# Performance work log

Hardware: AMD Instinct MI355X
Metric: run time of the kernel (lower is better)

The kernel has to match this reference:

```python
import jax, jax.numpy as jnp
import numpy as np

B, S, SE, D, H, F1, I, E, ND = 8, 512, 512, 1024, 16, 4096, 1024, 8, 4

def _ln(x, g, b, eps=1e-5):
    mu = x.mean(-1, keepdims=True)
    var = ((x - mu) ** 2).mean(-1, keepdims=True)
    return (x - mu) * jax.lax.rsqrt(var + eps) * g + b

def _mha(q_in, kv_in, qw, qb, kw, kb, vw, vb, ow, ob):
    b, sq, d = q_in.shape
    sk = kv_in.shape[1]
    dh = d // H
    scale = dh ** -0.5
    q = ((q_in @ qw.T + qb) * scale).reshape(b, sq, H, dh)
    k = (kv_in @ kw.T + kb).reshape(b, sk, H, dh)
    v = (kv_in @ vw.T + vb).reshape(b, sk, H, dh)
    attn = jax.nn.softmax(jnp.einsum('bqhd,bkhd->bhqk', q, k), axis=-1)
    o = jnp.einsum('bhqk,bkhd->bqhd', attn, v).reshape(b, sq, d)
    return o @ ow.T + ob

def setup_inputs():
    key = jax.random.key(0)
    ks = jax.random.split(key, 40)
    p = lambda i, sh: jax.random.normal(ks[i], sh, jnp.float32) * 0.02
    return {
        'hidden_states': jax.random.normal(ks[0], (B, S, D), jnp.float32),
        'encoder_hidden_states': jax.random.normal(ks[1], (B, SE, D), jnp.float32),
        'idxes': jax.random.randint(ks[2], (B,), 0, ND),
        'sa_qw': p(3, (D, D)), 'sa_qb': p(4, (D,)), 'sa_kw': p(5, (D, D)), 'sa_kb': p(6, (D,)),
        'sa_vw': p(7, (D, D)), 'sa_vb': p(8, (D,)), 'sa_ow': p(9, (D, D)), 'sa_ob': p(10, (D,)),
        'ca_qw': p(11, (D, D)), 'ca_qb': p(12, (D,)), 'ca_kw': p(13, (D, D)), 'ca_kb': p(14, (D,)),
        'ca_vw': p(15, (D, D)), 'ca_vb': p(16, (D,)), 'ca_ow': p(17, (D, D)), 'ca_ob': p(18, (D,)),
        'sa_ln_g': jnp.ones((D,), jnp.float32), 'sa_ln_b': jnp.zeros((D,), jnp.float32),
        'ca_ln_g': jnp.ones((D,), jnp.float32), 'ca_ln_b': jnp.zeros((D,), jnp.float32),
        'fin_ln_g': jnp.ones((D,), jnp.float32), 'fin_ln_b': jnp.zeros((D,), jnp.float32),
        'fc1_w': p(19, (F1, D)), 'fc1_b': p(20, (F1,)),
        'fc2_w': p(21, (D, F1)), 'fc2_b': p(22, (D,)),
        'exp1_w': p(23, (E, I, D)), 'exp1_b': p(24, (E, I)),
        'exp2_w': p(25, (E, D, I)),
        'gate_w': p(26, (ND, E, D)), 'gate_b': p(27, (ND, E)),
    }

def reference(hidden_states, encoder_hidden_states, idxes, sa_qw, sa_qb, sa_kw, sa_kb, sa_vw, sa_vb, sa_ow, sa_ob, ca_qw, ca_qb, ca_kw, ca_kb, ca_vw, ca_vb, ca_ow, ca_ob, sa_ln_g, sa_ln_b, ca_ln_g, ca_ln_b, fin_ln_g, fin_ln_b, fc1_w, fc1_b, fc2_w, fc2_b, exp1_w, exp1_b, exp2_w, gate_w, gate_b):
    # self-attention block
    res = hidden_states
    h = _mha(hidden_states, hidden_states, sa_qw, sa_qb, sa_kw, sa_kb, sa_vw, sa_vb, sa_ow, sa_ob)
    h = _ln(res + h, sa_ln_g, sa_ln_b)
    # cross-attention block
    res = h
    h = _mha(h, encoder_hidden_states, ca_qw, ca_qb, ca_kw, ca_kb, ca_vw, ca_vb, ca_ow, ca_ob)
    h = _ln(res + h, ca_ln_g, ca_ln_b)
    # dataset-gated MoE FFN (dropout=0 eval, margin_loss=False, keep_resident=True)
    bsz, seq, d = h.shape
    x = h.reshape(-1, d)                              # [T, D]
    tok_ds = jnp.repeat(idxes, seq)                   # [T] dataset id per token
    logits = jnp.einsum('ted,td->te', gate_w[tok_ds], x) + gate_b[tok_ds]
    probs = jax.nn.softmax(logits, axis=-1)
    gate = jnp.argmax(probs, axis=-1)                 # top-1 expert per token
    gate_value = jnp.max(probs, axis=-1)
    oh = jax.nn.one_hot(gate, E, dtype=x.dtype)       # [T, E] dispatch mask
    # effective expert fc1 = concat(fc1, expert_fc1): shared half + per-token expert half
    h1 = jax.nn.gelu(x @ fc1_w.T + fc1_b, approximate=False)                                  # [T, F1]
    h2 = jax.nn.gelu(jnp.einsum('td,te,eid->ti', x, oh, exp1_w) + exp1_b[gate], approximate=False)  # [T, I]
    # effective expert fc2 = concat(fc2, expert_fc2, dim=1), shared fc2 bias
    out = h1 @ fc2_w.T + jnp.einsum('ti,te,edi->td', h2, oh, exp2_w) + fc2_b                  # [T, D]
    out = out * gate_value[:, None]                   # keep_resident: scale before residual
    out = _ln(x + out, fin_ln_g, fin_ln_b)
    return out.reshape(bsz, seq, d)
```

## Files before the change

kernel.cpp:

```cpp
#include <hip/hip_runtime.h>
#include <math.h>

constexpr int cS = 512, cD = 1024, cH = 16, cDH = 64;
constexpr int cF1 = 4096, cI = 1024, cE = 8;
constexpr int cT = 4096;
constexpr long long TD = (long long)cT * cD;
constexpr long long WW = 1048576;

typedef __attribute__((ext_vector_type(8))) short bfrag;
typedef _Float16 f16x8 __attribute__((ext_vector_type(8)));
typedef __attribute__((ext_vector_type(4))) float f32x4;

__device__ __forceinline__ float gelu_exact(float x) {
  return 0.5f * x * (1.0f + erff(x * 0.70710678118654752440f));
}
__device__ __forceinline__ unsigned short f2b_rne(float x) {
  union { float f; unsigned u; } v; v.f = x;
  unsigned r = v.u + 0x7fffu + ((v.u >> 16) & 1u);
  return (unsigned short)(r >> 16);
}
__device__ __forceinline__ void split2(float v, unsigned short& h, unsigned short& m) {
  _Float16 hh = (_Float16)v;
  float r = v - (float)hh;
  _Float16 mm = (_Float16)r;
  union { _Float16 f; unsigned short u; } a, b;
  a.f = hh; b.f = mm;
  h = a.u; m = b.u;
}
__device__ __forceinline__ void async16(const void* g, void* l) {
  __builtin_amdgcn_global_load_lds(
      (const __attribute__((address_space(1))) unsigned int*)g,
      (__attribute__((address_space(3))) unsigned int*)l, 16, 0, 0);
}
__device__ __forceinline__ float wsum(float v) {
#pragma unroll
  for (int off = 32; off; off >>= 1) v += __shfl_xor(v, off, 64);
  return v;
}
__device__ __forceinline__ float wmax(float v) {
#pragma unroll
  for (int off = 32; off; off >>= 1) v = fmaxf(v, __shfl_xor(v, off, 64));
  return v;
}

template<int BM, int BN, int OUT_MODE>
__global__ __launch_bounds__(256) void mgemm2(
    const unsigned short* __restrict__ Ap, long long aPS, long long sA, int lda,
    const unsigned short* __restrict__ Bp, long long bPS, long long sB, int ldb,
    const float* __restrict__ bias,
    void* __restrict__ Cp, long long sC, int ldc,
    int K, float alpha, int zbase)
{
  constexpr int WM = BM / 2, WN = BN / 2, AI = WM / 16, BJ = WN / 16;
  constexpr int CA = 2 * (BM / 16);
  constexpr int CB = 2 * (BN / 16);
  constexpr int CTOT = CA + CB;
  static_assert(CTOT % 4 == 0, "chunk count");
  constexpr int NCH = CTOT / 4;
  constexpr int LT = (BM + BN) * 64;

  __shared__ unsigned short lds[2][LT];

  const int tid = threadIdx.x;
  const int w = tid >> 6, lane = tid & 63;
  const int z = blockIdx.z;
  const int m0 = blockIdx.x * BM, n0 = blockIdx.y * BN;
  const int wm = (w >> 1) * WM, wn = (w & 1) * WN;
  const int lr = lane >> 2, lc8 = (lane & 3) * 8;

  const unsigned short* gsrc[NCH];
  int loff[NCH];
#pragma unroll
  for (int ci = 0; ci < NCH; ++ci) {
    const int c = w + ci * 4;
    if (c < CA) {
      const int p = c / (BM / 16), cc = c % (BM / 16);
      const int row = cc * 16 + lr;
      gsrc[ci] = Ap + p * aPS + (long long)z * sA + (long long)(m0 + row) * lda + lc8;
      loff[ci] = p * (BM * 32) + cc * (16 * 32);
    } else {
      const int cb = c - CA;
      const int p = cb / (BN / 16), cc = cb % (BN / 16);
      const int row = cc * 16 + lr;
      gsrc[ci] = Bp + p * bPS + (long long)z * sB + (long long)(n0 + row) * ldb + lc8;
      loff[ci] = 2 * (BM * 32) + p * (BN * 32) + cc * (16 * 32);
    }
  }

  f32x4 acc[AI][BJ];
#pragma unroll
  for (int i = 0; i < AI; ++i)
#pragma unroll
    for (int j = 0; j < BJ; ++j) acc[i][j] = (f32x4){0.f, 0.f, 0.f, 0.f};

#pragma unroll
  for (int ci = 0; ci < NCH; ++ci) async16(gsrc[ci], &lds[0][loff[ci]]);
  __syncthreads();

  int cur = 0;
  for (int k0 = 32; k0 <= K; k0 += 32) {
    if (k0 < K) {
#pragma unroll
      for (int ci = 0; ci < NCH; ++ci) async16(gsrc[ci] + k0, &lds[cur ^ 1][loff[ci]]);
    }
    const unsigned short* LA0 = &lds[cur][0];
    const unsigned short* LA1 = &lds[cur][BM * 32];
    const unsigned short* LB0 = &lds[cur][2 * (BM * 32)];
    const unsigned short* LB1 = &lds[cur][2 * (BM * 32) + BN * 32];

    f16x8 bf0[BJ], bf1[BJ], af[AI];
#pragma unroll
    for (int j = 0; j < BJ; ++j) {
      bf0[j] = *(const f16x8*)&LB0[(wn + j * 16 + (lane & 15)) * 32 + (lane >> 4) * 8];
      bf1[j] = *(const f16x8*)&LB1[(wn + j * 16 + (lane & 15)) * 32 + (lane >> 4) * 8];
    }
#pragma unroll
    for (int i = 0; i < AI; ++i)
      af[i] = *(const f16x8*)&LA0[(wm + i * 16 + (lane & 15)) * 32 + (lane >> 4) * 8];
#pragma unroll
    for (int i = 0; i < AI; ++i)
#pragma unroll
      for (int j = 0; j < BJ; ++j)
        acc[i][j] = __builtin_amdgcn_mfma_f32_16x16x32_f16(af[i], bf0[j], acc[i][j], 0, 0, 0);
#pragma unroll
    for (int i = 0; i < AI; ++i)
#pragma unroll
      for (int j = 0; j < BJ; ++j)
        acc[i][j] = __builtin_amdgcn_mfma_f32_16x16x32_f16(af[i], bf1[j], acc[i][j], 0, 0, 0);
#pragma unroll
    for (int i = 0; i < AI; ++i)
      af[i] = *(const f16x8*)&LA1[(wm + i * 16 + (lane & 15)) * 32 + (lane >> 4) * 8];
#pragma unroll
    for (int i = 0; i < AI; ++i)
#pragma unroll
      for (int j = 0; j < BJ; ++j)
        acc[i][j] = __builtin_amdgcn_mfma_f32_16x16x32_f16(af[i], bf0[j], acc[i][j], 0, 0, 0);
    __syncthreads();
    cur ^= 1;
  }

  const int zz = zbase + z;
#pragma unroll
  for (int i = 0; i < AI; ++i) {
#pragma unroll
    for (int r = 0; r < 4; ++r) {
      const int gm = m0 + wm + i * 16 + (lane >> 4) * 4 + r;
#pragma unroll
      for (int j = 0; j < BJ; ++j) {
        const int gn = n0 + wn + j * 16 + (lane & 15);
        float v = acc[i][j][r];
        if constexpr (OUT_MODE == 4) {
          v += bias[zz * cD + gn];
          unsigned short* C = (unsigned short*)Cp + (long long)zz * 2 * TD;
          const int b = gm >> 9, s = gm & 511, h = gn >> 6, dd = gn & 63;
          const long long idx = (((long long)(b * cH + h) * cS + s) << 6) + dd;
          unsigned short h_, m_;
          split2(v, h_, m_);
          C[idx] = h_; C[TD + idx] = m_;
        } else if constexpr (OUT_MODE == 5) {
          const int b = zz >> 4, h = zz & 15;
          const long long idx = ((long long)(b * cS + gm) << 10) + h * 64 + gn;
          unsigned short h_, m_;
          split2(v, h_, m_);
          ((unsigned short*)Cp)[idx] = h_;
          ((unsigned short*)Cp)[sC + idx] = m_;
        } else {
          if (bias) v += bias[gn];
          v *= alpha;
          const long long idx = (long long)z * sC + (long long)gm * ldc + gn;
          ((float*)Cp)[idx] = v;
        }
      }
    }
  }
}

__global__ __launch_bounds__(256) void transposeV(
    const unsigned short* __restrict__ src, unsigned short* __restrict__ dst)
{
  __shared__ unsigned short t[128 * 64];
  const int st = blockIdx.x;
  const int bh = blockIdx.y;
  const long long pl = (long long)blockIdx.z * TD;
  const unsigned short* Sp = src + pl + ((long long)bh * cS + st * 128) * cDH;
  const int tid = threadIdx.x;
  const int r0 = tid >> 3, c0 = (tid & 7) * 8;
#pragma unroll
  for (int i = 0; i < 4; ++i) {
    const int r = r0 + i * 32;
    uint4 v = *(const uint4*)(Sp + (long long)r * cDH + c0);
    *(uint4*)&t[r * 64 + (c0 ^ ((r & 7) << 3))] = v;
  }
  __syncthreads();
  const int dd = tid >> 2;
  unsigned short* Dp = dst + pl + (long long)(bh * cDH + dd) * cS + st * 128;
#pragma unroll
  for (int i = 0; i < 4; ++i) {
    const int s0 = ((tid & 3) + i * 4) * 8;
    alignas(16) unsigned short v[8];
#pragma unroll
    for (int j = 0; j < 8; ++j)
      v[j] = t[(s0 + j) * 64 + (dd ^ (j << 3))];
    *(uint4*)(Dp + s0) = *(const uint4*)v;
  }
}

template<int GATHER>
__global__ __launch_bounds__(256) void mgemm1(
    const unsigned short* __restrict__ A, int lda,
    const unsigned short* __restrict__ Bw, long long sB, int ldb,
    const float* __restrict__ bias, int sBias,
    void* __restrict__ Cp, int ldc,
    int K, int act, int obf, int accum,
    const int* __restrict__ token_list, const int* __restrict__ offsets)
{
  int m0, n0, beg = 0, cnt = 0x7fffffff;
  long long boff = 0;
  if constexpr (GATHER) {
    const int e = blockIdx.y;
    beg = offsets[e]; cnt = offsets[e + 1] - beg;
    m0 = blockIdx.z * 128;
    if (m0 >= cnt) return;
    n0 = blockIdx.x * 128;
    boff = (long long)e * sB;
    if (bias) bias += (long long)e * sBias;
  } else {
    m0 = blockIdx.x * 128; n0 = blockIdx.y * 128;
  }
  __shared__ unsigned short lds[2][256 * 32];
  const int tid = threadIdx.x, w = tid >> 6, lane = tid & 63;
  const int wm = (w >> 1) * 64, wn = (w & 1) * 64;
  const int lr = lane >> 2, lc8 = (lane & 3) * 8;

  const unsigned short* gsrc[4];
  int loff[4];
#pragma unroll
  for (int ci = 0; ci < 4; ++ci) {
    const int c = w + ci * 4;
    if (c < 8) {
      const int row = c * 16 + lr;
      long long grow;
      if constexpr (GATHER) {
        int mr = m0 + row; if (mr >= cnt) mr = cnt - 1;
        grow = token_list[beg + mr];
      } else grow = m0 + row;
      gsrc[ci] = A + grow * (long long)lda + lc8;
      loff[ci] = c * (16 * 32);
    } else {
      const int cc = c - 8;
      const int row = cc * 16 + lr;
      gsrc[ci] = Bw + boff + (long long)(n0 + row) * ldb + lc8;
      loff[ci] = 128 * 32 + cc * (16 * 32);
    }
  }
  f32x4 acc[4][4];
#pragma unroll
  for (int i = 0; i < 4; ++i)
#pragma unroll
    for (int j = 0; j < 4; ++j) acc[i][j] = (f32x4){0.f, 0.f, 0.f, 0.f};

#pragma unroll
  for (int ci = 0; ci < 4; ++ci) async16(gsrc[ci], &lds[0][loff[ci]]);
  __syncthreads();

  int cur = 0;
  for (int k0 = 32; k0 <= K; k0 += 32) {
    if (k0 < K) {
#pragma unroll
      for (int ci = 0; ci < 4; ++ci) async16(gsrc[ci] + k0, &lds[cur ^ 1][loff[ci]]);
    }
    const unsigned short* lA = &lds[cur][0];
    const unsigned short* lB = &lds[cur][128 * 32];
    bfrag af[4], bf[4];
#pragma unroll
    for (int i = 0; i < 4; ++i)
      af[i] = *(const bfrag*)&lA[(wm + i * 16 + (lane & 15)) * 32 + (lane >> 4) * 8];
#pragma unroll
    for (int j = 0; j < 4; ++j)
      bf[j] = *(const bfrag*)&lB[(wn + j * 16 + (lane & 15)) * 32 + (lane >> 4) * 8];
#pragma unroll
    for (int i = 0; i < 4; ++i)
#pragma unroll
      for (int j = 0; j < 4; ++j)
        acc[i][j] = __builtin_amdgcn_mfma_f32_16x16x32_bf16(af[i], bf[j], acc[i][j], 0, 0, 0);
    __syncthreads();
    cur ^= 1;
  }

#pragma unroll
  for (int i = 0; i < 4; ++i) {
#pragma unroll
    for (int r = 0; r < 4; ++r) {
      const int ml = wm + i * 16 + (lane >> 4) * 4 + r;
      long long orow = 0; bool ok = true;
      if constexpr (GATHER) {
        if (m0 + ml < cnt) orow = token_list[beg + m0 + ml]; else ok = false;
      } else orow = m0 + ml;
      if (ok) {
#pragma unroll
        for (int j = 0; j < 4; ++j) {
          const int gn = n0 + wn + j * 16 + (lane & 15);
          float v = acc[i][j][r];
          if (bias) v += bias[gn];
          if (act) v = gelu_exact(v);
          const long long idx = orow * (long long)ldc + gn;
          if (obf) ((unsigned short*)Cp)[idx] = f2b_rne(v);
          else if (accum) ((float*)Cp)[idx] += v;
          else ((float*)Cp)[idx] = v;
        }
      }
    }
  }
}

__global__ __launch_bounds__(256) void softmax2(
    const float* __restrict__ Sc, unsigned short* __restrict__ P, long long pPS)
{
  const int w = threadIdx.x >> 6, lane = threadIdx.x & 63;
  const long long row = (long long)blockIdx.x * 4 + w;
  const float* pr = Sc + row * cS + lane * 8;
  float4 a = *(const float4*)pr;
  float4 b = *(const float4*)(pr + 4);
  float e[8] = {a.x, a.y, a.z, a.w, b.x, b.y, b.z, b.w};
  float m = e[0];
#pragma unroll
  for (int q = 1; q < 8; ++q) m = fmaxf(m, e[q]);
  m = wmax(m);
  float s = 0.f;
#pragma unroll
  for (int q = 0; q < 8; ++q) { e[q] = expf(e[q] - m); s += e[q]; }
  s = wsum(s);
  const float inv = 1.0f / s;
  unsigned h[4], mm[4];
#pragma unroll
  for (int q = 0; q < 4; ++q) {
    unsigned short h0, m0s, h1, m1s;
    split2(e[2 * q] * inv, h0, m0s);
    split2(e[2 * q + 1] * inv, h1, m1s);
    h[q] = (unsigned)h0 | ((unsigned)h1 << 16);
    mm[q] = (unsigned)m0s | ((unsigned)m1s << 16);
  }
  const long long o = row * cS + lane * 8;
  *(uint4*)&P[o] = *(const uint4*)h;
  *(uint4*)&P[pPS + o] = *(const uint4*)mm;
}

__global__ __launch_bounds__(256) void addln_kernel(
    const float* __restrict__ ra, const float* __restrict__ rb,
    const float* __restrict__ rowscale,
    const float* __restrict__ g, const float* __restrict__ be,
    float* __restrict__ out, unsigned short* __restrict__ out16,
    unsigned short* __restrict__ out2p,
    int gate_on, const int* __restrict__ idxes,
    const float* __restrict__ gw, const float* __restrict__ gb,
    int* __restrict__ gate_idx, float* __restrict__ gate_val, int* __restrict__ counts)
{
  const int w = threadIdx.x >> 6, lane = threadIdx.x & 63;
  const int row = blockIdx.x * 4 + w;
  const long long base = (long long)row * cD + lane * 16;
  const float sc = rowscale ? rowscale[row] : 1.0f;
  float v[16];
#pragma unroll
  for (int q = 0; q < 4; ++q) {
    float4 a = *(const float4*)(ra + base + q * 4);
    float4 b = *(const float4*)(rb + base + q * 4);
    v[q * 4 + 0] = a.x + b.x * sc; v[q * 4 + 1] = a.y + b.y * sc;
    v[q * 4 + 2] = a.z + b.z * sc; v[q * 4 + 3] = a.w + b.w * sc;
  }
  float s = 0.f;
#pragma unroll
  for (int q = 0; q < 16; ++q) s += v[q];
  const float mu = wsum(s) * (1.0f / cD);
  float vp = 0.f;
#pragma unroll
  for (int q = 0; q < 16; ++q) { float c = v[q] - mu; vp += c * c; }
  const float rstd = 1.0f / sqrtf(wsum(vp) * (1.0f / cD) + 1e-5f);
  float x[16];
#pragma unroll
  for (int q = 0; q < 4; ++q) {
    float4 gv = *(const float4*)(g + lane * 16 + q * 4);
    float4 bv = *(const float4*)(be + lane * 16 + q * 4);
    x[q * 4 + 0] = (v[q * 4 + 0] - mu) * rstd * gv.x + bv.x;
    x[q * 4 + 1] = (v[q * 4 + 1] - mu) * rstd * gv.y + bv.y;
    x[q * 4 + 2] = (v[q * 4 + 2] - mu) * rstd * gv.z + bv.z;
    x[q * 4 + 3] = (v[q * 4 + 3] - mu) * rstd * gv.w + bv.w;
  }
  if (out) {
#pragma unroll
    for (int q = 0; q < 4; ++q) {
      float4 o; o.x = x[q * 4]; o.y = x[q * 4 + 1]; o.z = x[q * 4 + 2]; o.w = x[q * 4 + 3];
      *(float4*)(out + base + q * 4) = o;
    }
  }
  if (out16) {
    unsigned u[8];
#pragma unroll
    for (int q = 0; q < 8; ++q)
      u[q] = (unsigned)f2b_rne(x[2 * q]) | ((unsigned)f2b_rne(x[2 * q + 1]) << 16);
    *(uint4*)&out16[base] = *(const uint4*)&u[0];
    *(uint4*)&out16[base + 8] = *(const uint4*)&u[4];
  }
  if (out2p) {
    unsigned uh[8], um[8];
#pragma unroll
    for (int q = 0; q < 8; ++q) {
      unsigned short h0, m0s, h1, m1s;
      split2(x[2 * q], h0, m0s);
      split2(x[2 * q + 1], h1, m1s);
      uh[q] = (unsigned)h0 | ((unsigned)h1 << 16);
      um[q] = (unsigned)m0s | ((unsigned)m1s << 16);
    }
    *(uint4*)&out2p[base] = *(const uint4*)&uh[0];
    *(uint4*)&out2p[base + 8] = *(const uint4*)&uh[4];
    *(uint4*)&out2p[TD + base] = *(const uint4*)&um[0];
    *(uint4*)&out2p[TD + base + 8] = *(const uint4*)&um[4];
  }
  if (gate_on) {
    const int ds = idxes[row >> 9];
    const float* gwr = gw + (long long)ds * (cE * cD) + lane * 16;
    float glog[8];
#pragma unroll
    for (int e = 0; e < 8; ++e) {
      float pe = 0.f;
#pragma unroll
      for (int q = 0; q < 4; ++q) {
        float4 wv = *(const float4*)(gwr + e * cD + q * 4);
        pe += x[q * 4] * wv.x + x[q * 4 + 1] * wv.y + x[q * 4 + 2] * wv.z + x[q * 4 + 3] * wv.w;
      }
      glog[e] = wsum(pe);
    }
    if (lane == 0) {
      float m = glog[0] + gb[ds * cE];
      int arg = 0;
      float gl[8];
      gl[0] = m;
#pragma unroll
      for (int e = 1; e < 8; ++e) {
        gl[e] = glog[e] + gb[ds * cE + e];
        if (gl[e] > m) { m = gl[e]; arg = e; }
      }
      float ssum = 0.f;
#pragma unroll
      for (int e = 0; e < 8; ++e) ssum += expf(gl[e] - m);
      gate_idx[row] = arg;
      gate_val[row] = 1.0f / ssum;
      atomicAdd(&counts[arg], 1);
    }
  }
}

__global__ __launch_bounds__(256) void conv2x4(
    const float* s0, const float* s1, const float* s2, const float* s3,
    unsigned short* dst, int n, float sc0)
{
  const int wsel = blockIdx.y;
  const float* s = (wsel == 0) ? s0 : (wsel == 1) ? s1 : (wsel == 2) ? s2 : s3;
  const float sc = (wsel == 0) ? sc0 : 1.0f;
  unsigned short* d = dst + (long long)wsel * 2 * n;
  const long long i = ((long long)blockIdx.x * 256 + threadIdx.x) * 4;
  if (i >= n) return;
  float4 v = *(const float4*)(s + i);
  float vv[4] = {v.x * sc, v.y * sc, v.z * sc, v.w * sc};
  unsigned short h[4], m[4];
#pragma unroll
  for (int q = 0; q < 4; ++q) split2(vv[q], h[q], m[q]);
  uint2 u;
  u.x = (unsigned)h[0] | ((unsigned)h[1] << 16); u.y = (unsigned)h[2] | ((unsigned)h[3] << 16);
  *(uint2*)&d[i] = u;
  u.x = (unsigned)m[0] | ((unsigned)m[1] << 16); u.y = (unsigned)m[2] | ((unsigned)m[3] << 16);
  *(uint2*)&d[n + i] = u;
}

__global__ __launch_bounds__(256) void conv2p(const float* __restrict__ s,
                                              unsigned short* __restrict__ d, long long n)
{
  const long long i = ((long long)blockIdx.x * 256 + threadIdx.x) * 4;
  if (i >= n) return;
  float4 v = *(const float4*)(s + i);
  unsigned short h[4], m[4];
  split2(v.x, h[0], m[0]); split2(v.y, h[1], m[1]);
  split2(v.z, h[2], m[2]); split2(v.w, h[3], m[3]);
  uint2 u;
  u.x = (unsigned)h[0] | ((unsigned)h[1] << 16); u.y = (unsigned)h[2] | ((unsigned)h[3] << 16);
  *(uint2*)&d[i] = u;
  u.x = (unsigned)m[0] | ((unsigned)m[1] << 16); u.y = (unsigned)m[2] | ((unsigned)m[3] << 16);
  *(uint2*)&d[n + i] = u;
}

__global__ __launch_bounds__(256) void conv1(const float* __restrict__ s,
                                             unsigned short* __restrict__ d, long long n)
{
  const long long i = ((long long)blockIdx.x * 256 + threadIdx.x) * 4;
  if (i >= n) return;
  float4 v = *(const float4*)(s + i);
  uint2 u;
  u.x = (unsigned)f2b_rne(v.x) | ((unsigned)f2b_rne(v.y) << 16);
  u.y = (unsigned)f2b_rne(v.z) | ((unsigned)f2b_rne(v.w) << 16);
  *(uint2*)&d[i] = u;
}

__global__ void prep_bias(const float* a0, const float* a1, const float* a2,
                          const float* b0, const float* b1, const float* b2,
                          float* dst)
{
  const int i = blockIdx.x * 256 + threadIdx.x;
  const int seg = i >> 10, off = i & 1023;
  const float* srcs[6] = {a0, a1, a2, b0, b1, b2};
  const float sc = (seg == 0 || seg == 3) ? 0.125f : 1.0f;
  dst[i] = srcs[seg][off] * sc;
}

__global__ void scan_kernel(const int* __restrict__ counts, int* __restrict__ offsets,
                            int* __restrict__ cursor)
{
  if (threadIdx.x == 0 && blockIdx.x == 0) {
    int a = 0;
    for (int e = 0; e < cE; ++e) { offsets[e] = a; cursor[e] = a; a += counts[e]; }
    offsets[cE] = a;
  }
}

__global__ __launch_bounds__(256) void scatter_kernel(
    const int* __restrict__ gate_idx, int* __restrict__ cursor, int* __restrict__ token_list)
{
  int t = blockIdx.x * 256 + threadIdx.x;
  if (t < cT) {
    int e = gate_idx[t];
    int slot = atomicAdd(&cursor[e], 1);
    token_list[slot] = t;
  }
}

extern "C" void kernel_launch(void* const* d_in, const int* in_sizes, int n_in,
                              void* d_out, int out_size, void* d_ws, size_t ws_size,
                              hipStream_t stream)
{
  (void)in_sizes; (void)n_in; (void)out_size;
  const float* hidden  = (const float*)d_in[0];
  const float* encoder = (const float*)d_in[1];
  const int*   idxes   = (const int*)d_in[2];
  const float* sa_qw = (const float*)d_in[3];
  const float* sa_qb = (const float*)d_in[4];
  const float* sa_kw = (const float*)d_in[5];
  const float* sa_kb = (const float*)d_in[6];
  const float* sa_vw = (const float*)d_in[7];
  const float* sa_vb = (const float*)d_in[8];
  const float* sa_ow = (const float*)d_in[9];
  const float* sa_ob = (const float*)d_in[10];
  const float* ca_qw = (const float*)d_in[11];
  const float* ca_qb = (const float*)d_in[12];
  const float* ca_kw = (const float*)d_in[13];
  const float* ca_kb = (const float*)d_in[14];
  const float* ca_vw = (const float*)d_in[15];
  const float* ca_vb = (const float*)d_in[16];
  const float* ca_ow = (const float*)d_in[17];
  const float* ca_ob = (const float*)d_in[18];
  const float* sa_ln_g = (const float*)d_in[19];
  const float* sa_ln_b = (const float*)d_in[20];
  const float* ca_ln_g = (const float*)d_in[21];
  const float* ca_ln_b = (const float*)d_in[22];
  const float* fin_ln_g = (const float*)d_in[23];
  const float* fin_ln_b = (const float*)d_in[24];
  const float* fc1_w = (const float*)d_in[25];
  const float* fc1_b = (const float*)d_in[26];
  const float* fc2_w = (const float*)d_in[27];
  const float* fc2_b = (const float*)d_in[28];
  const float* exp1_w = (const float*)d_in[29];
  const float* exp1_b = (const float*)d_in[30];
  const float* exp2_w = (const float*)d_in[31];
  const float* gate_w = (const float*)d_in[32];
  const float* gate_b = (const float*)d_in[33];
  float* out = (float*)d_out;

  size_t off = 0;
  auto alloc = [&](size_t bytes) {
    void* p = (char*)d_ws + off;
    off += (bytes + 255) & ~(size_t)255;
    return p;
  };
  unsigned short* wbuf = (unsigned short*)alloc(4ll * 2 * WW * 2);
  unsigned short* QKVs = (unsigned short*)alloc(4ll * 2 * TD * 2);
  unsigned short* attnO16 = (unsigned short*)alloc(2ll * TD * 2);
  float* hsa   = (float*)alloc(TD * 4);
  float* biasb = (float*)alloc(6 * cD * 4);
  float* gate_val = (float*)alloc(cT * 4);
  int* gate_idx   = (int*)alloc(cT * 4);
  int* token_list = (int*)alloc(cT * 4);
  int* ctl        = (int*)alloc(64 * 4);
  int* counts  = ctl;
  int* offsets = ctl + 16;
  int* cursor  = ctl + 32;
  const size_t off_x = off;
  float* xbuf = (float*)alloc(TD * 4);
  unsigned short* x16 = (unsigned short*)alloc(TD * 2);

  long long region_bytes = (long long)ws_size - (long long)off_x;
  long long perz = (long long)cS * cS * 8;
  int ZB = (int)(region_bytes / perz);
  if (ZB < 1) ZB = 1;
  if (ZB > 128) ZB = 128;
  float* scoresF = (float*)((char*)d_ws + off_x);
  unsigned short* Pp = (unsigned short*)((char*)d_ws + off_x + (long long)ZB * cS * cS * 4);
  const long long pPS = (long long)ZB * cS * cS;

  unsigned short* A16 = QKVs + 6 * TD;
  unsigned short* hsa16 = attnO16;
  float* OdeltaF = (float*)QKVs;
  unsigned short* h1 = attnO16;
  unsigned short* h2 = QKVs;
  float* moeF = (float*)(QKVs + 2 * WW * 4);

  dim3 blk(256);
  hipMemsetAsync(counts, 0, cE * sizeof(int), stream);
  prep_bias<<<dim3(24), blk, 0, stream>>>(sa_qb, sa_kb, sa_vb, ca_qb, ca_kb, ca_vb, biasb);

  auto attention = [&]() {
    for (int zb = 0; zb < 128; zb += ZB) {
      int zc = 128 - zb; if (zc > ZB) zc = ZB;
      mgemm2<128, 64, 0><<<dim3(4, 8, zc), blk, 0, stream>>>(
          QKVs + (long long)zb * (cS * cDH), TD, (long long)cS * cDH, cDH,
          QKVs + 2 * TD + (long long)zb * (cS * cDH), TD, (long long)cS * cDH, cDH,
          nullptr, scoresF, (long long)cS * cS, cS, cDH, 1.0f, 0);
      softmax2<<<dim3(zc * cS / 4), blk, 0, stream>>>(scoresF, Pp, pPS);
      mgemm2<128, 64, 5><<<dim3(4, 1, zc), blk, 0, stream>>>(
          Pp, pPS, (long long)cS * cS, cS,
          QKVs + 6 * TD + (long long)zb * (cDH * cS), TD, (long long)cDH * cS, cS,
          nullptr, attnO16, TD, 0, cS, 1.0f, zb);
    }
  };

  conv2x4<<<dim3(1024, 4), blk, 0, stream>>>(sa_qw, sa_kw, sa_vw, sa_ow, wbuf, (int)WW, 0.125f);
  conv2p<<<dim3(4096), blk, 0, stream>>>(hidden, A16, TD);
  mgemm2<64, 128, 4><<<dim3(64, 8, 3), blk, 0, stream>>>(
      A16, TD, 0, cD, wbuf, WW, 2 * WW, cD,
      biasb, QKVs, 0, 0, cD, 1.0f, 0);
  transposeV<<<dim3(4, 128, 2), blk, 0, stream>>>(QKVs + 4 * TD, QKVs + 6 * TD);
  attention();
  mgemm2<64, 128, 0><<<dim3(64, 8, 1), blk, 0, stream>>>(
      attnO16, TD, 0, cD, wbuf + 6ll * WW, WW, 0, cD,
      sa_ob, OdeltaF, 0, cD, cD, 1.0f, 0);
  addln_kernel<<<dim3(cT / 4), blk, 0, stream>>>(
      hidden, OdeltaF, nullptr, sa_ln_g, sa_ln_b, hsa, nullptr, hsa16,
      0, nullptr, nullptr, nullptr, nullptr, nullptr, nullptr);

  conv2x4<<<dim3(1024, 4), blk, 0, stream>>>(ca_qw, ca_kw, ca_vw, ca_ow, wbuf, (int)WW, 0.125f);
  mgemm2<64, 128, 4><<<dim3(64, 8, 1), blk, 0, stream>>>(
      hsa16, TD, 0, cD, wbuf, WW, 2 * WW, cD,
      biasb + 3 * cD, QKVs, 0, 0, cD, 1.0f, 0);
  conv2p<<<dim3(4096), blk, 0, stream>>>(encoder, A16, TD);
  mgemm2<64, 128, 4><<<dim3(64, 8, 2), blk, 0, stream>>>(
      A16, TD, 0, cD, wbuf + 2ll * WW, WW, 2 * WW, cD,
      biasb + 3 * cD, QKVs, 0, 0, cD, 1.0f, 1);
  transposeV<<<dim3(4, 128, 2), blk, 0, stream>>>(QKVs + 4 * TD, QKVs + 6 * TD);
  attention();
  mgemm2<64, 128, 0><<<dim3(64, 8, 1), blk, 0, stream>>>(
      attnO16, TD, 0, cD, wbuf + 6ll * WW, WW, 0, cD,
      ca_ob, OdeltaF, 0, cD, cD, 1.0f, 0);
  addln_kernel<<<dim3(cT / 4), blk, 0, stream>>>(
      hsa, OdeltaF, nullptr, ca_ln_g, ca_ln_b, xbuf, x16, nullptr,
      1, idxes, gate_w, gate_b, gate_idx, gate_val, counts);

  scan_kernel<<<dim3(1), dim3(64), 0, stream>>>(counts, offsets, cursor);
  scatter_kernel<<<dim3(16), blk, 0, stream>>>(gate_idx, cursor, token_list);

  unsigned short* wfc1 = wbuf;
  unsigned short* wfc2 = wbuf + 4194304;
  conv1<<<dim3(4096), blk, 0, stream>>>(fc1_w, wfc1, 4194304);
  conv1<<<dim3(4096), blk, 0, stream>>>(fc2_w, wfc2, 4194304);
  for (int tc = 0; tc < cT; tc += 2048) {
    mgemm1<0><<<dim3(16, 32), blk, 0, stream>>>(
        x16 + (long long)tc * cD, cD, wfc1, 0, cD, fc1_b, 0,
        h1, cF1, cD, 1, 1, 0, nullptr, nullptr);
    mgemm1<0><<<dim3(16, 8), blk, 0, stream>>>(
        h1, cF1, wfc2, 0, cF1, fc2_b, 0,
        moeF + (long long)tc * cD, cD, cF1, 0, 0, 0, nullptr, nullptr);
  }
  conv1<<<dim3(8192), blk, 0, stream>>>(exp1_w, wbuf, 8388608);
  mgemm1<1><<<dim3(8, 8, 32), blk, 0, stream>>>(
      x16, cD, wbuf, (long long)cI * cD, cD, exp1_b, cI,
      h2, cI, cD, 1, 1, 0, token_list, offsets);
  conv1<<<dim3(8192), blk, 0, stream>>>(exp2_w, wbuf, 8388608);
  mgemm1<1><<<dim3(8, 8, 32), blk, 0, stream>>>(
      h2, cI, wbuf, (long long)cD * cI, cI, nullptr, 0,
      moeF, cD, cI, 0, 0, 1, token_list, offsets);

  addln_kernel<<<dim3(cT / 4), blk, 0, stream>>>(
      xbuf, moeF, gate_val, fin_ln_g, fin_ln_b, out, nullptr, nullptr,
      0, nullptr, nullptr, nullptr, nullptr, nullptr, nullptr);
}
```

Measured before the change: 1.207 ms.

## Generalize GEMM warp layout, enlarge tiles, and run FFN in one pass

Adds template parameters for warp count and warp-row arrangement to the split-precision GEMM kernel. Projection GEMMs switch to larger tiles, including 128x256 tiles with 512-thread blocks, and the QK^T scores GEMM uses 64x256 tiles. The point is to raise data reuse per block and cut the number of launched blocks. The shared FFN is no longer chunked in two 2048-token passes; it runs as a single pass with h1 moved to a larger buffer region, which adds memory-footprint risk if that region overlaps other live data.

```diff
diff --git a/kernel.cpp b/kernel.cpp
--- a/kernel.cpp
+++ b/kernel.cpp
@@ -43,20 +43,21 @@
   return v;
 }
 
-template<int BM, int BN, int OUT_MODE>
-__global__ __launch_bounds__(256) void mgemm2(
+template<int BM, int BN, int NW, int WR, int OUT_MODE>
+__global__ __launch_bounds__(NW * 64) void mgemm2(
     const unsigned short* __restrict__ Ap, long long aPS, long long sA, int lda,
     const unsigned short* __restrict__ Bp, long long bPS, long long sB, int ldb,
     const float* __restrict__ bias,
     void* __restrict__ Cp, long long sC, int ldc,
     int K, float alpha, int zbase)
 {
-  constexpr int WM = BM / 2, WN = BN / 2, AI = WM / 16, BJ = WN / 16;
+  constexpr int WC = NW / WR;
+  constexpr int WM = BM / WR, WN = BN / WC, AI = WM / 16, BJ = WN / 16;
   constexpr int CA = 2 * (BM / 16);
   constexpr int CB = 2 * (BN / 16);
   constexpr int CTOT = CA + CB;
-  static_assert(CTOT % 4 == 0, "chunk count");
-  constexpr int NCH = CTOT / 4;
+  static_assert(CTOT % NW == 0, "chunk count");
+  constexpr int NCH = CTOT / NW;
   constexpr int LT = (BM + BN) * 64;
 
   __shared__ unsigned short lds[2][LT];
@@ -65,14 +66,14 @@
   const int w = tid >> 6, lane = tid & 63;
   const int z = blockIdx.z;
   const int m0 = blockIdx.x * BM, n0 = blockIdx.y * BN;
-  const int wm = (w >> 1) * WM, wn = (w & 1) * WN;
+  const int wm = (w / WC) * WM, wn = (w % WC) * WN;
   const int lr = lane >> 2, lc8 = (lane & 3) * 8;
 
   const unsigned short* gsrc[NCH];
   int loff[NCH];
 #pragma unroll
   for (int ci = 0; ci < NCH; ++ci) {
-    const int c = w + ci * 4;
+    const int c = w + ci * NW;
     if (c < CA) {
       const int p = c / (BM / 16), cc = c % (BM / 16);
       const int row = cc * 16 + lr;
@@ -606,23 +607,23 @@
   unsigned short* A16 = QKVs + 6 * TD;
   unsigned short* hsa16 = attnO16;
   float* OdeltaF = (float*)QKVs;
-  unsigned short* h1 = attnO16;
   unsigned short* h2 = QKVs;
   float* moeF = (float*)(QKVs + 2 * WW * 4);
-
-  dim3 blk(256);
+  unsigned short* h1 = QKVs + 16ll * WW;
+
+  dim3 blk(256), blk512(512);
   hipMemsetAsync(counts, 0, cE * sizeof(int), stream);
   prep_bias<<<dim3(24), blk, 0, stream>>>(sa_qb, sa_kb, sa_vb, ca_qb, ca_kb, ca_vb, biasb);
 
   auto attention = [&]() {
     for (int zb = 0; zb < 128; zb += ZB) {
       int zc = 128 - zb; if (zc > ZB) zc = ZB;
-      mgemm2<128, 64, 0><<<dim3(4, 8, zc), blk, 0, stream>>>(
+      mgemm2<64, 256, 4, 1, 0><<<dim3(8, 2, zc), blk, 0, stream>>>(
           QKVs + (long long)zb * (cS * cDH), TD, (long long)cS * cDH, cDH,
           QKVs + 2 * TD + (long long)zb * (cS * cDH), TD, (long long)cS * cDH, cDH,
           nullptr, scoresF, (long long)cS * cS, cS, cDH, 1.0f, 0);
       softmax2<<<dim3(zc * cS / 4), blk, 0, stream>>>(scoresF, Pp, pPS);
-      mgemm2<128, 64, 5><<<dim3(4, 1, zc), blk, 0, stream>>>(
+      mgemm2<128, 64, 4, 2, 5><<<dim3(4, 1, zc), blk, 0, stream>>>(
           Pp, pPS, (long long)cS * cS, cS,
           QKVs + 6 * TD + (long long)zb * (cDH * cS), TD, (long long)cDH * cS, cS,
           nullptr, attnO16, TD, 0, cS, 1.0f, zb);
@@ -631,12 +632,12 @@
 
   conv2x4<<<dim3(1024, 4), blk, 0, stream>>>(sa_qw, sa_kw, sa_vw, sa_ow, wbuf, (int)WW, 0.125f);
   conv2p<<<dim3(4096), blk, 0, stream>>>(hidden, A16, TD);
-  mgemm2<64, 128, 4><<<dim3(64, 8, 3), blk, 0, stream>>>(
+  mgemm2<128, 256, 8, 2, 4><<<dim3(32, 4, 3), blk512, 0, stream>>>(
       A16, TD, 0, cD, wbuf, WW, 2 * WW, cD,
       biasb, QKVs, 0, 0, cD, 1.0f, 0);
   transposeV<<<dim3(4, 128, 2), blk, 0, stream>>>(QKVs + 4 * TD, QKVs + 6 * TD);
   attention();
-  mgemm2<64, 128, 0><<<dim3(64, 8, 1), blk, 0, stream>>>(
+  mgemm2<64, 256, 4, 1, 0><<<dim3(64, 4, 1), blk, 0, stream>>>(
       attnO16, TD, 0, cD, wbuf + 6ll * WW, WW, 0, cD,
       sa_ob, OdeltaF, 0, cD, cD, 1.0f, 0);
   addln_kernel<<<dim3(cT / 4), blk, 0, stream>>>(
@@ -644,16 +645,16 @@
       0, nullptr, nullptr, nullptr, nullptr, nullptr, nullptr);
 
   conv2x4<<<dim3(1024, 4), blk, 0, stream>>>(ca_qw, ca_kw, ca_vw, ca_ow, wbuf, (int)WW, 0.125f);
-  mgemm2<64, 128, 4><<<dim3(64, 8, 1), blk, 0, stream>>>(
+  mgemm2<64, 256, 4, 1, 4><<<dim3(64, 4, 1), blk, 0, stream>>>(
       hsa16, TD, 0, cD, wbuf, WW, 2 * WW, cD,
       biasb + 3 * cD, QKVs, 0, 0, cD, 1.0f, 0);
   conv2p<<<dim3(4096), blk, 0, stream>>>(encoder, A16, TD);
-  mgemm2<64, 128, 4><<<dim3(64, 8, 2), blk, 0, stream>>>(
+  mgemm2<128, 256, 8, 2, 4><<<dim3(32, 4, 2), blk512, 0, stream>>>(
       A16, TD, 0, cD, wbuf + 2ll * WW, WW, 2 * WW, cD,
       biasb + 3 * cD, QKVs, 0, 0, cD, 1.0f, 1);
   transposeV<<<dim3(4, 128, 2), blk, 0, stream>>>(QKVs + 4 * TD, QKVs + 6 * TD);
   attention();
-  mgemm2<64, 128, 0><<<dim3(64, 8, 1), blk, 0, stream>>>(
+  mgemm2<64, 256, 4, 1, 0><<<dim3(64, 4, 1), blk, 0, stream>>>(
       attnO16, TD, 0, cD, wbuf + 6ll * WW, WW, 0, cD,
       ca_ob, OdeltaF, 0, cD, cD, 1.0f, 0);
   addln_kernel<<<dim3(cT / 4), blk, 0, stream>>>(
@@ -667,14 +668,12 @@
   unsigned short* wfc2 = wbuf + 4194304;
   conv1<<<dim3(4096), blk, 0, stream>>>(fc1_w, wfc1, 4194304);
   conv1<<<dim3(4096), blk, 0, stream>>>(fc2_w, wfc2, 4194304);
-  for (int tc = 0; tc < cT; tc += 2048) {
-    mgemm1<0><<<dim3(16, 32), blk, 0, stream>>>(
-        x16 + (long long)tc * cD, cD, wfc1, 0, cD, fc1_b, 0,
-        h1, cF1, cD, 1, 1, 0, nullptr, nullptr);
-    mgemm1<0><<<dim3(16, 8), blk, 0, stream>>>(
-        h1, cF1, wfc2, 0, cF1, fc2_b, 0,
-        moeF + (long long)tc * cD, cD, cF1, 0, 0, 0, nullptr, nullptr);
-  }
+  mgemm1<0><<<dim3(32, 32), blk, 0, stream>>>(
+      x16, cD, wfc1, 0, cD, fc1_b, 0,
+      h1, cF1, cD, 1, 1, 0, nullptr, nullptr);
+  mgemm1<0><<<dim3(32, 8), blk, 0, stream>>>(
+      h1, cF1, wfc2, 0, cF1, fc2_b, 0,
+      moeF, cD, cF1, 0, 0, 0, nullptr, nullptr);
   conv1<<<dim3(8192), blk, 0, stream>>>(exp1_w, wbuf, 8388608);
   mgemm1<1><<<dim3(8, 8, 32), blk, 0, stream>>>(
       x16, cD, wbuf, (long long)cI * cD, cD, exp1_b, cI,
```

Measured after the change: 1.155 ms. 4.4% less time.
